# Performance work log

Measured on AMD Instinct MI355X. Metric: run time of the kernel, lower is better.

## Reference

```python
import jax, jax.numpy as jnp
import numpy as np

N_NODES = 100000
N_EDGES = 3200000
D_IN = 256
D_HID = 256
D_OUT = 64


def setup_inputs() -> dict:
    key = jax.random.key(0)
    k1, k2, k3, k4 = jax.random.split(key, 4)
    x = jax.random.normal(k1, (N_NODES, D_IN), dtype=jnp.float32)
    edge_index = jax.random.randint(k2, (2, N_EDGES), 0, N_NODES, dtype=jnp.int32)
    W1 = jax.random.normal(k3, (D_IN, D_HID), dtype=jnp.float32) / np.sqrt(D_IN)
    b1 = jnp.zeros((D_HID,), dtype=jnp.float32)
    W2 = jax.random.normal(k4, (D_HID, D_OUT), dtype=jnp.float32) / np.sqrt(D_HID)
    b2 = jnp.zeros((D_OUT,), dtype=jnp.float32)
    return {"x": x, "edge_index": edge_index, "W1": W1, "b1": b1, "W2": W2, "b2": b2}


def _gcn_conv(x, src, dst, norm, W, b, n_nodes):
    # dense linear transform, then normalized scatter-add aggregation
    h = x @ W  # [N, out]
    msg = norm[:, None] * h[src]  # gather + scale, [E+N, out]
    out = jax.ops.segment_sum(msg, dst, num_segments=n_nodes)
    return out + b


def reference(x, edge_index, W1, b1, W2, b2):
    n = x.shape[0]
    # add self-loops (PyG GCNConv default)
    loops = jnp.arange(n, dtype=edge_index.dtype)
    src = jnp.concatenate([edge_index[0], loops])
    dst = jnp.concatenate([edge_index[1], loops])
    # symmetric normalization deg^{-1/2}[src] * deg^{-1/2}[dst]
    deg = jax.ops.segment_sum(jnp.ones_like(src, dtype=x.dtype), dst, num_segments=n)
    dinv = jnp.where(deg > 0, jax.lax.rsqrt(jnp.maximum(deg, 1.0)), 0.0)
    norm = dinv[src] * dinv[dst]

    h = _gcn_conv(x, src, dst, norm, W1, b1, n)
    h = jax.nn.relu(h)
    # dropout is identity at inference
    h = _gcn_conv(h, src, dst, norm, W2, b2, n)
    return jax.nn.log_softmax(h, axis=1)
```

## Files before the change

kernel.cpp:

```cpp
#include <hip/hip_runtime.h>
#include <hip/hip_bf16.h>


typedef __bf16 bf16;
typedef bf16 bf16x8 __attribute__((ext_vector_type(8)));
typedef float f32x4 __attribute__((ext_vector_type(4)));
typedef float f32x2 __attribute__((ext_vector_type(2)));

#define NBLK 256

__global__ __launch_bounds__(256) void k_b1(const int* __restrict__ edge, int E, int chunk,
                                            int NB, int* __restrict__ gcnt) {
    __shared__ int cnt[512];
    int tid = threadIdx.x;
    for (int i = tid; i < NB; i += 256) cnt[i] = 0;
    __syncthreads();
    int s = blockIdx.x * chunk, e = min(s + chunk, E);
    for (int i = s + tid; i < e; i += 256) atomicAdd(&cnt[edge[E + i] >> 9], 1);
    __syncthreads();
    for (int i = tid; i < NB; i += 256) gcnt[blockIdx.x * NB + i] = cnt[i];
}

__global__ void k_b2(const int* __restrict__ gcnt, int NB, int E, int* __restrict__ bstart) {
    __shared__ int col[256];
    int k = threadIdx.x;
    int sum = 0;
    if (k < NB)
        for (int b = 0; b < NBLK; ++b) sum += gcnt[b * NB + k];
    col[k] = sum;
    __syncthreads();
    for (int o = 1; o < 256; o <<= 1) {
        int v = (k >= o) ? col[k - o] : 0;
        __syncthreads();
        col[k] += v;
        __syncthreads();
    }
    if (k < NB) bstart[k] = col[k] - sum;
    if (k == 0) bstart[NB] = E;
}

__global__ void k_b2b(int* __restrict__ gcnt, int NB, const int* __restrict__ bstart) {
    __shared__ int col[256];
    int b = threadIdx.x;
    int k = blockIdx.x;
    int v = gcnt[b * NB + k];
    col[b] = v;
    __syncthreads();
    for (int o = 1; o < 256; o <<= 1) {
        int t = (b >= o) ? col[b - o] : 0;
        __syncthreads();
        col[b] += t;
        __syncthreads();
    }
    gcnt[b * NB + k] = bstart[k] + col[b] - v;
}

__global__ __launch_bounds__(256) void k_b3(const int* __restrict__ edge, int E, int chunk,
                                            int NB, const int* __restrict__ base,
                                            int* __restrict__ ebuf) {
    __shared__ int cnt[512];
    __shared__ int bs[512];
    int tid = threadIdx.x;
    for (int i = tid; i < NB; i += 256) {
        cnt[i] = 0;
        bs[i] = base[blockIdx.x * NB + i];
    }
    __syncthreads();
    int s = blockIdx.x * chunk, e = min(s + chunk, E);
    for (int i = s + tid; i < e; i += 256) {
        int sv = edge[i], dv = edge[E + i];
        int k = dv >> 9;
        int r = atomicAdd(&cnt[k], 1);
        ebuf[bs[k] + r] = sv | ((dv & 511) << 17);
    }
}

__global__ __launch_bounds__(256) void k_b45(const int* __restrict__ ebuf,
                                             const int* __restrict__ bstart,
                                             const float* __restrict__ scale, int n, int E,
                                             int NB, int* __restrict__ off,
                                             float* __restrict__ dinv,
                                             float* __restrict__ ws) {
    __shared__ int cnt[512];
    __shared__ int red[256];
    int tid = threadIdx.x;
    int k = blockIdx.x;
    cnt[tid] = 0;
    cnt[tid + 256] = 0;
    __syncthreads();
    int s = bstart[k], e = bstart[k + 1];
    for (int i = s + tid; i < e; i += 256) atomicAdd(&cnt[(ebuf[i] >> 17) & 511], 1);
    __syncthreads();
    int c0 = cnt[tid * 2], c1 = cnt[tid * 2 + 1];
    int sum = c0 + c1;
    red[tid] = sum;
    __syncthreads();
    for (int o = 1; o < 256; o <<= 1) {
        int v = (tid >= o) ? red[tid - o] : 0;
        __syncthreads();
        red[tid] += v;
        __syncthreads();
    }
    int ex = red[tid] - sum;
    int base = k << 9;
    int g0 = base + tid * 2, g1 = g0 + 1;
    int o0 = s + ex, o1 = s + ex + c0;
    if (g0 < n) {
        off[g0] = o0;
        float d0 = rsqrtf((float)(c0 + 1));
        dinv[g0] = d0;
        ws[g0] = d0 * scale[g0];
    } else if (g0 == n) off[g0] = o0;
    if (g1 < n) {
        off[g1] = o1;
        float d1 = rsqrtf((float)(c1 + 1));
        dinv[g1] = d1;
        ws[g1] = d1 * scale[g1];
    } else if (g1 == n) off[g1] = o1;
    if (k == NB - 1 && tid == 0) off[n] = E;
}

__global__ __launch_bounds__(256) void k_b6(const int* __restrict__ ebuf,
                                            const int* __restrict__ bstart,
                                            const int* __restrict__ off,
                                            const float* __restrict__ ws, int n,
                                            int2* __restrict__ pair) {
    __shared__ int cnt[512];
    __shared__ int offl[512];
    int tid = threadIdx.x;
    int k = blockIdx.x;
    int base = k << 9;
    cnt[tid] = 0;
    cnt[tid + 256] = 0;
    offl[tid] = (base + tid < n) ? off[base + tid] : 0;
    offl[tid + 256] = (base + 256 + tid < n) ? off[base + 256 + tid] : 0;
    __syncthreads();
    int s = bstart[k], e = bstart[k + 1];
    for (int i = s + tid; i < e; i += 256) {
        int pk = ebuf[i];
        int sv = pk & 0x1ffff;
        int node = (pk >> 17) & 511;
        int r = atomicAdd(&cnt[node], 1);
        pair[offl[node] + r] = make_int2(sv << 8, __float_as_int(ws[sv]));
    }
}

__global__ __launch_bounds__(256) void k_quant(const float* __restrict__ x,
                                               unsigned char* __restrict__ xq,
                                               float* __restrict__ scale, int n) {
    int row = blockIdx.x * 4 + (threadIdx.x >> 6);
    int lane = threadIdx.x & 63;
    if (row >= n) return;
    f32x4 v = ((const f32x4*)x)[(size_t)row * 64 + lane];
    float m = fmaxf(fmaxf(fabsf(v[0]), fabsf(v[1])), fmaxf(fabsf(v[2]), fabsf(v[3])));
    for (int o = 32; o > 0; o >>= 1) m = fmaxf(m, __shfl_xor(m, o));
    m = fmaxf(m, 1e-20f);
    float inv = 127.0f / m;
    int b0 = (__float2int_rn(v[0] * inv) + 128) & 255;
    int b1 = (__float2int_rn(v[1] * inv) + 128) & 255;
    int b2 = (__float2int_rn(v[2] * inv) + 128) & 255;
    int b3 = (__float2int_rn(v[3] * inv) + 128) & 255;
    ((int*)xq)[(size_t)row * 64 + lane] = b0 | (b1 << 8) | (b2 << 16) | (b3 << 24);
    if (lane == 0) scale[row] = m / 127.0f;
}

__global__ __launch_bounds__(256) void k_quant2(const bf16* __restrict__ tb,
                                                const float* __restrict__ dinv,
                                                unsigned char* __restrict__ tq,
                                                float* __restrict__ w2v, int n) {
    int t = blockIdx.x * 256 + threadIdx.x;
    int row = t >> 3;
    int l8 = t & 7;
    if (row >= n) return;
    bf16x8 v = ((const bf16x8*)tb)[(size_t)row * 8 + l8];
    float f[8], m = 0.0f;
#pragma unroll
    for (int j = 0; j < 8; ++j) { f[j] = (float)v[j]; m = fmaxf(m, fabsf(f[j])); }
    for (int o = 4; o > 0; o >>= 1) m = fmaxf(m, __shfl_xor(m, o));
    m = fmaxf(m, 1e-20f);
    float inv = 127.0f / m;
    int lo = 0, hi = 0;
#pragma unroll
    for (int j = 0; j < 4; ++j) lo |= ((__float2int_rn(f[j] * inv) + 128) & 255) << (8 * j);
#pragma unroll
    for (int j = 0; j < 4; ++j) hi |= ((__float2int_rn(f[4 + j] * inv) + 128) & 255) << (8 * j);
    ((int2*)tq)[(size_t)row * 8 + l8] = make_int2(lo, hi);
    if (l8 == 0) w2v[row] = dinv[row] * (m / 127.0f);
}

__global__ void k_wt(const float* __restrict__ W, bf16* __restrict__ Wt, int NC) {
    int nc = blockIdx.x;
    int k = threadIdx.x;
    Wt[nc * 256 + k] = (bf16)W[k * NC + nc];
}

__device__ __forceinline__ void acc16(f32x2 a[8], uint4 t, float w, float& wsum) {
    wsum += w;
    f32x2 w2 = {w, w};
    unsigned u0 = t.x, u1 = t.y, u2 = t.z, u3 = t.w;
    f32x2 c;
    c[0] = (float)(u0 & 255u);         c[1] = (float)((u0 >> 8) & 255u);  a[0] += w2 * c;
    c[0] = (float)((u0 >> 16) & 255u); c[1] = (float)(u0 >> 24);         a[1] += w2 * c;
    c[0] = (float)(u1 & 255u);         c[1] = (float)((u1 >> 8) & 255u);  a[2] += w2 * c;
    c[0] = (float)((u1 >> 16) & 255u); c[1] = (float)(u1 >> 24);         a[3] += w2 * c;
    c[0] = (float)(u2 & 255u);         c[1] = (float)((u2 >> 8) & 255u);  a[4] += w2 * c;
    c[0] = (float)((u2 >> 16) & 255u); c[1] = (float)(u2 >> 24);         a[5] += w2 * c;
    c[0] = (float)(u3 & 255u);         c[1] = (float)((u3 >> 8) & 255u);  a[6] += w2 * c;
    c[0] = (float)((u3 >> 16) & 255u); c[1] = (float)(u3 >> 24);         a[7] += w2 * c;
}

__device__ __forceinline__ void acc8(f32x2 a[4], int2 t, float w, float& wsum) {
    wsum += w;
    f32x2 w2 = {w, w};
    unsigned u0 = (unsigned)t.x, u1 = (unsigned)t.y;
    f32x2 c;
    c[0] = (float)(u0 & 255u);         c[1] = (float)((u0 >> 8) & 255u);  a[0] += w2 * c;
    c[0] = (float)((u0 >> 16) & 255u); c[1] = (float)(u0 >> 24);         a[1] += w2 * c;
    c[0] = (float)(u1 & 255u);         c[1] = (float)((u1 >> 8) & 255u);  a[2] += w2 * c;
    c[0] = (float)((u1 >> 16) & 255u); c[1] = (float)(u1 >> 24);         a[3] += w2 * c;
}

__global__ __launch_bounds__(256) void k_agg1(const unsigned char* __restrict__ xq,
                                              const float* __restrict__ wsv,
                                              const int* __restrict__ off,
                                              const int2* __restrict__ pair,
                                              const float* __restrict__ dinv,
                                              bf16* __restrict__ ax, int n) {
    int wv = blockIdx.x * 4 + (threadIdx.x >> 6);
    int lane = threadIdx.x & 63;
    int node = wv * 4 + (lane >> 4);
    int l16 = lane & 15;
    if (node >= n) return;
    int s0 = off[node], s1 = off[node + 1];
    float dv = dinv[node];
    const unsigned char* xqb = xq + l16 * 16;
    f32x2 a[8] = {};
    float wsum = 0.0f;
    uint4 xs = *(const uint4*)(xqb + (size_t)node * 256);
    acc16(a, xs, wsv[node], wsum);
    int e = s0;
    if (s1 - s0 >= 8) {
        int2 p[8];
#pragma unroll
        for (int q = 0; q < 8; ++q) p[q] = pair[s0 + q];
        e = s0 + 8;
        for (; e + 8 <= s1; e += 8) {
            uint4 t[8];
#pragma unroll
            for (int q = 0; q < 8; ++q)
                t[q] = *(const uint4*)(xqb + (unsigned)p[q].x);
            int2 pn[8];
#pragma unroll
            for (int q = 0; q < 8; ++q) pn[q] = pair[e + q];
#pragma unroll
            for (int q = 0; q < 8; ++q) acc16(a, t[q], __int_as_float(p[q].y), wsum);
#pragma unroll
            for (int q = 0; q < 8; ++q) p[q] = pn[q];
        }
        uint4 t[8];
#pragma unroll
        for (int q = 0; q < 8; ++q)
            t[q] = *(const uint4*)(xqb + (unsigned)p[q].x);
#pragma unroll
        for (int q = 0; q < 8; ++q) acc16(a, t[q], __int_as_float(p[q].y), wsum);
    }
    for (; e < s1; ++e) {
        int2 p = pair[e];
        uint4 t = *(const uint4*)(xqb + (unsigned)p.x);
        acc16(a, t, __int_as_float(p.y), wsum);
    }
    float c = 128.0f * wsum;
    bf16x8 o0, o1;
#pragma unroll
    for (int j = 0; j < 4; ++j) {
        o0[2 * j]     = (bf16)((a[j][0] - c) * dv);
        o0[2 * j + 1] = (bf16)((a[j][1] - c) * dv);
        o1[2 * j]     = (bf16)((a[4 + j][0] - c) * dv);
        o1[2 * j + 1] = (bf16)((a[4 + j][1] - c) * dv);
    }
    ((bf16x8*)ax)[(size_t)node * 32 + l16 * 2] = o0;
    ((bf16x8*)ax)[(size_t)node * 32 + l16 * 2 + 1] = o1;
}

__device__ __forceinline__ int swz(int s) { return s ^ ((s >> 3) & 7); }

__global__ __launch_bounds__(256) void k_gemmp(const bf16* __restrict__ A,
                                               const bf16* __restrict__ Bt,
                                               const float* __restrict__ bias,
                                               bf16* __restrict__ C, int n) {
    __shared__ __align__(16) bf16 As[4 * 64 * 8];
    __shared__ __align__(16) bf16 Bs[16 * 64 * 8];
    int tid = threadIdx.x;
    int bm = blockIdx.x * 64;
    int w = tid >> 6, lane = tid & 63;

    int r = tid >> 2;
    int cq = tid & 3;
    int a_slot = swz(((r >> 4) * 64) + cq * 16 + (r & 15));
    int arow = bm + r; if (arow > n - 1) arow = n - 1;

    f32x4 acc[16] = {};

    for (int k0 = 0; k0 < 256; k0 += 32) {
        __syncthreads();
        uint4 av = *(const uint4*)(A + (size_t)arow * 256 + k0 + cq * 8);
        *(uint4*)(As + a_slot * 8) = av;
#pragma unroll
        for (int rep = 0; rep < 4; ++rep) {
            int r2 = rep * 64 + r;
            uint4 bv = *(const uint4*)(Bt + (size_t)r2 * 256 + k0 + cq * 8);
            *(uint4*)(Bs + swz(((r2 >> 4) * 64) + cq * 16 + (r2 & 15)) * 8) = bv;
        }
        __syncthreads();
        bf16x8 af = *(const bf16x8*)(As + swz(w * 64 + lane) * 8);
#pragma unroll
        for (int ct = 0; ct < 16; ++ct) {
            bf16x8 bfr = *(const bf16x8*)(Bs + swz(ct * 64 + lane) * 8);
            acc[ct] = __builtin_amdgcn_mfma_f32_16x16x32_bf16(af, bfr, acc[ct], 0, 0, 0);
        }
    }

    int colb = lane & 15, rowq = lane >> 4;
#pragma unroll
    for (int ct = 0; ct < 16; ++ct) {
        int col = ct * 16 + colb;
        float bv = bias[col];
#pragma unroll
        for (int rr = 0; rr < 4; ++rr) {
            int row = bm + w * 16 + rowq * 4 + rr;
            if (row < n) {
                float v = acc[ct][rr] + bv;
                C[(size_t)row * 256 + col] = (bf16)(v > 0.0f ? v : 0.0f);
            }
        }
    }
}

__global__ __launch_bounds__(256) void k_gemm2(const bf16* __restrict__ A,
                                               const bf16* __restrict__ Bt,
                                               bf16* __restrict__ C, int n) {
    __shared__ __align__(16) bf16 As[4 * 64 * 8];
    __shared__ __align__(16) bf16 Bs[4 * 64 * 8];
    int tid = threadIdx.x;
    int bm = blockIdx.x * 64;
    int w = tid >> 6, lane = tid & 63;
    int wm = w >> 1, wn = w & 1;

    int r = tid >> 2;
    int cq = tid & 3;
    int lds_slot = swz(((r >> 4) * 64) + cq * 16 + (r & 15));
    int arow = bm + r; if (arow > n - 1) arow = n - 1;

    f32x4 acc[2][2] = {};

    for (int k0 = 0; k0 < 256; k0 += 32) {
        __syncthreads();
        uint4 av = *(const uint4*)(A + (size_t)arow * 256 + k0 + cq * 8);
        uint4 bv = *(const uint4*)(Bt + (size_t)r * 256 + k0 + cq * 8);
        *(uint4*)(As + lds_slot * 8) = av;
        *(uint4*)(Bs + lds_slot * 8) = bv;
        __syncthreads();
#pragma unroll
        for (int i = 0; i < 2; ++i) {
            bf16x8 af = *(const bf16x8*)(As + swz((wm * 2 + i) * 64 + lane) * 8);
#pragma unroll
            for (int j = 0; j < 2; ++j) {
                bf16x8 bfr = *(const bf16x8*)(Bs + swz((wn * 2 + j) * 64 + lane) * 8);
                acc[i][j] = __builtin_amdgcn_mfma_f32_16x16x32_bf16(af, bfr, acc[i][j], 0, 0, 0);
            }
        }
    }

    int colb = lane & 15, rowq = lane >> 4;
#pragma unroll
    for (int i = 0; i < 2; ++i) {
#pragma unroll
        for (int j = 0; j < 2; ++j) {
            int col = wn * 32 + j * 16 + colb;
#pragma unroll
            for (int rr = 0; rr < 4; ++rr) {
                int row = bm + wm * 32 + i * 16 + rowq * 4 + rr;
                if (row < n) C[(size_t)row * 64 + col] = (bf16)acc[i][j][rr];
            }
        }
    }
}

__global__ __launch_bounds__(256) void k_agg2(const unsigned char* __restrict__ tq,
                                              const float* __restrict__ w2v,
                                              const int* __restrict__ off,
                                              const int2* __restrict__ pair,
                                              const float* __restrict__ dinv,
                                              const float* __restrict__ b2,
                                              float* __restrict__ out, int n) {
    int wv = blockIdx.x * 4 + (threadIdx.x >> 6);
    int lane = threadIdx.x & 63;
    int node = wv * 8 + (lane >> 3);
    int l8 = lane & 7;
    if (node >= n) return;
    int s0 = off[node], s1 = off[node + 1];
    float dv = dinv[node];
    const unsigned char* tqb = tq + l8 * 8;
    int2 ts = *(const int2*)(tqb + (size_t)node * 64);
    f32x2 a[4] = {};
    float wsum = 0.0f;
    acc8(a, ts, w2v[node], wsum);
    int e = s0;
    if (s1 - s0 >= 4) {
        int2 p[4]; float sc[4];
#pragma unroll
        for (int q = 0; q < 4; ++q) p[q] = pair[s0 + q];
#pragma unroll
        for (int q = 0; q < 4; ++q) sc[q] = w2v[(unsigned)p[q].x >> 8];
        e = s0 + 4;
        for (; e + 4 <= s1; e += 4) {
            int2 t[4];
#pragma unroll
            for (int q = 0; q < 4; ++q) t[q] = *(const int2*)(tqb + ((unsigned)p[q].x >> 2));
            int2 pn[4];
#pragma unroll
            for (int q = 0; q < 4; ++q) pn[q] = pair[e + q];
            float scn[4];
#pragma unroll
            for (int q = 0; q < 4; ++q) scn[q] = w2v[(unsigned)pn[q].x >> 8];
#pragma unroll
            for (int q = 0; q < 4; ++q) acc8(a, t[q], sc[q], wsum);
#pragma unroll
            for (int q = 0; q < 4; ++q) { p[q] = pn[q]; sc[q] = scn[q]; }
        }
        int2 t[4];
#pragma unroll
        for (int q = 0; q < 4; ++q) t[q] = *(const int2*)(tqb + ((unsigned)p[q].x >> 2));
#pragma unroll
        for (int q = 0; q < 4; ++q) acc8(a, t[q], sc[q], wsum);
    }
    for (; e < s1; ++e) {
        int2 p = pair[e];
        float w = w2v[(unsigned)p.x >> 8];
        int2 t = *(const int2*)(tqb + ((unsigned)p.x >> 2));
        acc8(a, t, w, wsum);
    }
    float c = 128.0f * wsum;
    float aa[8];
#pragma unroll
    for (int j = 0; j < 4; ++j) { aa[2 * j] = a[j][0]; aa[2 * j + 1] = a[j][1]; }
    const float4* B2 = (const float4*)b2;
    float4 bv0 = B2[l8 * 2], bv1 = B2[l8 * 2 + 1];
    aa[0] = (aa[0] - c) * dv + bv0.x; aa[1] = (aa[1] - c) * dv + bv0.y;
    aa[2] = (aa[2] - c) * dv + bv0.z; aa[3] = (aa[3] - c) * dv + bv0.w;
    aa[4] = (aa[4] - c) * dv + bv1.x; aa[5] = (aa[5] - c) * dv + bv1.y;
    aa[6] = (aa[6] - c) * dv + bv1.z; aa[7] = (aa[7] - c) * dv + bv1.w;
    float m = aa[0];
#pragma unroll
    for (int j = 1; j < 8; ++j) m = fmaxf(m, aa[j]);
    for (int o = 4; o > 0; o >>= 1) m = fmaxf(m, __shfl_xor(m, o));
    float s = 0.0f;
#pragma unroll
    for (int j = 0; j < 8; ++j) s += __expf(aa[j] - m);
    for (int o = 4; o > 0; o >>= 1) s += __shfl_xor(s, o);
    float ls = m + __logf(s);
    f32x4 o0, o1;
    o0[0] = aa[0] - ls; o0[1] = aa[1] - ls; o0[2] = aa[2] - ls; o0[3] = aa[3] - ls;
    o1[0] = aa[4] - ls; o1[1] = aa[5] - ls; o1[2] = aa[6] - ls; o1[3] = aa[7] - ls;
    f32x4* O = (f32x4*)out;
    O[(size_t)node * 16 + l8 * 2] = o0;
    O[(size_t)node * 16 + l8 * 2 + 1] = o1;
}

extern "C" void kernel_launch(void* const* d_in, const int* in_sizes, int n_in,
                              void* d_out, int out_size, void* d_ws, size_t ws_size,
                              hipStream_t stream) {
    const float* x   = (const float*)d_in[0];
    const int*  edge = (const int*)d_in[1];
    const float* W1  = (const float*)d_in[2];
    const float* b1  = (const float*)d_in[3];
    const float* W2  = (const float*)d_in[4];
    const float* b2  = (const float*)d_in[5];
    float* out = (float*)d_out;

    int n = in_sizes[0] / 256;
    int E = in_sizes[1] / 2;
    int NB = (n + 511) >> 9;
    int chunk = (E + NBLK - 1) / NBLK;

    char* ws = (char*)d_ws;
    auto alloc = [&](size_t bytes) -> char* {
        char* p = ws;
        ws += (bytes + 255) & ~(size_t)255;
        return p;
    };
    int*   gcnt   = (int*)alloc((size_t)NBLK * NB * 4);
    int*   bstart = (int*)alloc((size_t)(NB + 1) * 4);
    int*   ebuf   = (int*)alloc((size_t)E * 4);
    float* dinv   = (float*)alloc((size_t)n * 4);
    float* wsv    = (float*)alloc((size_t)n * 4);
    int*   off    = (int*)alloc((size_t)(n + 1) * 4);
    int2*  pair   = (int2*)alloc((size_t)E * 8);
    unsigned char* xq = (unsigned char*)alloc((size_t)n * 256);
    float* scale  = (float*)alloc((size_t)n * 4);
    bf16*  ax     = (bf16*)alloc((size_t)n * 256 * 2);
    bf16*  h1     = (bf16*)alloc((size_t)n * 256 * 2);
    bf16*  tb     = (bf16*)alloc((size_t)n * 64 * 2);
    unsigned char* tq = (unsigned char*)alloc((size_t)n * 64);
    float* w2v    = (float*)alloc((size_t)n * 4);
    bf16*  W1t    = (bf16*)alloc(256 * 256 * 2);
    bf16*  W2t    = (bf16*)alloc(64 * 256 * 2);

    k_quant<<<(n + 3) / 4, 256, 0, stream>>>(x, xq, scale, n);

    k_b1<<<NBLK, 256, 0, stream>>>(edge, E, chunk, NB, gcnt);
    k_b2<<<1, 256, 0, stream>>>(gcnt, NB, E, bstart);
    k_b2b<<<NB, 256, 0, stream>>>(gcnt, NB, bstart);
    k_b3<<<NBLK, 256, 0, stream>>>(edge, E, chunk, NB, gcnt, ebuf);
    k_b45<<<NB, 256, 0, stream>>>(ebuf, bstart, scale, n, E, NB, off, dinv, wsv);
    k_b6<<<NB, 256, 0, stream>>>(ebuf, bstart, off, wsv, n, pair);

    k_wt<<<256, 256, 0, stream>>>(W1, W1t, 256);
    k_wt<<<64, 256, 0, stream>>>(W2, W2t, 64);

    k_agg1<<<(n + 15) / 16, 256, 0, stream>>>(xq, wsv, off, pair, dinv, ax, n);
    k_gemmp<<<(n + 63) / 64, 256, 0, stream>>>(ax, W1t, b1, h1, n);

    k_gemm2<<<(n + 63) / 64, 256, 0, stream>>>(h1, W2t, tb, n);
    k_quant2<<<(n * 8 + 255) / 256, 256, 0, stream>>>(tb, dinv, tq, w2v, n);
    k_agg2<<<(n + 31) / 32, 256, 0, stream>>>(tq, w2v, off, pair, dinv, b2, out, n);
}
```

Measured before the change: 541.4 us.

## Retile layer-1 GEMM to 128-row blocks, deepen agg2 prefetch, merge weight transposes

The first GEMM now runs 512-thread blocks over 128 rows, and each wave computes a 64x64 output tile with a 4x4 MFMA register block, so LDS fragment loads are reused across more MFMAs. The layer-2 aggregation software pipeline is widened from 4 to 8 edges in flight to hide gather latency. The two weight-transpose launches are merged into one kernel. The changes raise register pressure in the GEMM and in agg2, which may lower occupancy, and nodes with fewer than 8 edges now go entirely through the scalar tail loop.

```diff
diff --git a/kernel.cpp b/kernel.cpp
--- a/kernel.cpp
+++ b/kernel.cpp
@@ -188,10 +188,12 @@
     if (l8 == 0) w2v[row] = dinv[row] * (m / 127.0f);
 }
 
-__global__ void k_wt(const float* __restrict__ W, bf16* __restrict__ Wt, int NC) {
-    int nc = blockIdx.x;
+__global__ void k_wt(const float* __restrict__ W1, const float* __restrict__ W2,
+                     bf16* __restrict__ W1t, bf16* __restrict__ W2t) {
+    int b = blockIdx.x;
     int k = threadIdx.x;
-    Wt[nc * 256 + k] = (bf16)W[k * NC + nc];
+    if (b < 256) W1t[b * 256 + k] = (bf16)W1[k * 256 + b];
+    else { int nc = b - 256; W2t[nc * 256 + k] = (bf16)W2[k * 64 + nc]; }
 }
 
 __device__ __forceinline__ void acc16(f32x2 a[8], uint4 t, float w, float& wsum) {
@@ -284,56 +286,66 @@
 
 __device__ __forceinline__ int swz(int s) { return s ^ ((s >> 3) & 7); }
 
-__global__ __launch_bounds__(256) void k_gemmp(const bf16* __restrict__ A,
+__global__ __launch_bounds__(512) void k_gemmp(const bf16* __restrict__ A,
                                                const bf16* __restrict__ Bt,
                                                const float* __restrict__ bias,
                                                bf16* __restrict__ C, int n) {
-    __shared__ __align__(16) bf16 As[4 * 64 * 8];
+    __shared__ __align__(16) bf16 As[8 * 64 * 8];
     __shared__ __align__(16) bf16 Bs[16 * 64 * 8];
     int tid = threadIdx.x;
-    int bm = blockIdx.x * 64;
+    int bm = blockIdx.x * 128;
     int w = tid >> 6, lane = tid & 63;
+    int wm = w >> 2;
+    int wn = w & 3;
 
     int r = tid >> 2;
     int cq = tid & 3;
     int a_slot = swz(((r >> 4) * 64) + cq * 16 + (r & 15));
     int arow = bm + r; if (arow > n - 1) arow = n - 1;
 
-    f32x4 acc[16] = {};
+    f32x4 acc[4][4] = {};
 
     for (int k0 = 0; k0 < 256; k0 += 32) {
         __syncthreads();
         uint4 av = *(const uint4*)(A + (size_t)arow * 256 + k0 + cq * 8);
         *(uint4*)(As + a_slot * 8) = av;
 #pragma unroll
-        for (int rep = 0; rep < 4; ++rep) {
-            int r2 = rep * 64 + r;
+        for (int rep = 0; rep < 2; ++rep) {
+            int r2 = rep * 128 + r;
             uint4 bv = *(const uint4*)(Bt + (size_t)r2 * 256 + k0 + cq * 8);
             *(uint4*)(Bs + swz(((r2 >> 4) * 64) + cq * 16 + (r2 & 15)) * 8) = bv;
         }
         __syncthreads();
-        bf16x8 af = *(const bf16x8*)(As + swz(w * 64 + lane) * 8);
-#pragma unroll
-        for (int ct = 0; ct < 16; ++ct) {
-            bf16x8 bfr = *(const bf16x8*)(Bs + swz(ct * 64 + lane) * 8);
-            acc[ct] = __builtin_amdgcn_mfma_f32_16x16x32_bf16(af, bfr, acc[ct], 0, 0, 0);
-        }
+        bf16x8 af[4], bfr[4];
+#pragma unroll
+        for (int i = 0; i < 4; ++i)
+            af[i] = *(const bf16x8*)(As + swz(((wm * 4 + i) * 64) + lane) * 8);
+#pragma unroll
+        for (int j = 0; j < 4; ++j)
+            bfr[j] = *(const bf16x8*)(Bs + swz(((wn * 4 + j) * 64) + lane) * 8);
+#pragma unroll
+        for (int i = 0; i < 4; ++i)
+#pragma unroll
+            for (int j = 0; j < 4; ++j)
+                acc[i][j] = __builtin_amdgcn_mfma_f32_16x16x32_bf16(af[i], bfr[j], acc[i][j], 0, 0, 0);
     }
 
     int colb = lane & 15, rowq = lane >> 4;
 #pragma unroll
-    for (int ct = 0; ct < 16; ++ct) {
-        int col = ct * 16 + colb;
-        float bv = bias[col];
-#pragma unroll
-        for (int rr = 0; rr < 4; ++rr) {
-            int row = bm + w * 16 + rowq * 4 + rr;
-            if (row < n) {
-                float v = acc[ct][rr] + bv;
-                C[(size_t)row * 256 + col] = (bf16)(v > 0.0f ? v : 0.0f);
+    for (int i = 0; i < 4; ++i)
+#pragma unroll
+        for (int j = 0; j < 4; ++j) {
+            int col = wn * 64 + j * 16 + colb;
+            float bv = bias[col];
+#pragma unroll
+            for (int rr = 0; rr < 4; ++rr) {
+                int row = bm + wm * 64 + i * 16 + rowq * 4 + rr;
+                if (row < n) {
+                    float v = acc[i][j][rr] + bv;
+                    C[(size_t)row * 256 + col] = (bf16)(v > 0.0f ? v : 0.0f);
+                }
             }
         }
-    }
 }
 
 __global__ __launch_bounds__(256) void k_gemm2(const bf16* __restrict__ A,
@@ -406,33 +418,33 @@
     float wsum = 0.0f;
     acc8(a, ts, w2v[node], wsum);
     int e = s0;
-    if (s1 - s0 >= 4) {
-        int2 p[4]; float sc[4];
-#pragma unroll
-        for (int q = 0; q < 4; ++q) p[q] = pair[s0 + q];
-#pragma unroll
-        for (int q = 0; q < 4; ++q) sc[q] = w2v[(unsigned)p[q].x >> 8];
-        e = s0 + 4;
-        for (; e + 4 <= s1; e += 4) {
-            int2 t[4];
-#pragma unroll
-            for (int q = 0; q < 4; ++q) t[q] = *(const int2*)(tqb + ((unsigned)p[q].x >> 2));
-            int2 pn[4];
-#pragma unroll
-            for (int q = 0; q < 4; ++q) pn[q] = pair[e + q];
-            float scn[4];
-#pragma unroll
-            for (int q = 0; q < 4; ++q) scn[q] = w2v[(unsigned)pn[q].x >> 8];
-#pragma unroll
-            for (int q = 0; q < 4; ++q) acc8(a, t[q], sc[q], wsum);
-#pragma unroll
-            for (int q = 0; q < 4; ++q) { p[q] = pn[q]; sc[q] = scn[q]; }
+    if (s1 - s0 >= 8) {
+        int2 p[8]; float sc[8];
+#pragma unroll
+        for (int q = 0; q < 8; ++q) p[q] = pair[s0 + q];
+#pragma unroll
+        for (int q = 0; q < 8; ++q) sc[q] = w2v[(unsigned)p[q].x >> 8];
+        e = s0 + 8;
+        for (; e + 8 <= s1; e += 8) {
+            int2 t[8];
+#pragma unroll
+            for (int q = 0; q < 8; ++q) t[q] = *(const int2*)(tqb + ((unsigned)p[q].x >> 2));
+            int2 pn[8];
+#pragma unroll
+            for (int q = 0; q < 8; ++q) pn[q] = pair[e + q];
+            float scn[8];
+#pragma unroll
+            for (int q = 0; q < 8; ++q) scn[q] = w2v[(unsigned)pn[q].x >> 8];
+#pragma unroll
+            for (int q = 0; q < 8; ++q) acc8(a, t[q], sc[q], wsum);
+#pragma unroll
+            for (int q = 0; q < 8; ++q) { p[q] = pn[q]; sc[q] = scn[q]; }
         }
-        int2 t[4];
-#pragma unroll
-        for (int q = 0; q < 4; ++q) t[q] = *(const int2*)(tqb + ((unsigned)p[q].x >> 2));
-#pragma unroll
-        for (int q = 0; q < 4; ++q) acc8(a, t[q], sc[q], wsum);
+        int2 t[8];
+#pragma unroll
+        for (int q = 0; q < 8; ++q) t[q] = *(const int2*)(tqb + ((unsigned)p[q].x >> 2));
+#pragma unroll
+        for (int q = 0; q < 8; ++q) acc8(a, t[q], sc[q], wsum);
     }
     for (; e < s1; ++e) {
         int2 p = pair[e];
@@ -515,11 +527,10 @@
     k_b45<<<NB, 256, 0, stream>>>(ebuf, bstart, scale, n, E, NB, off, dinv, wsv);
     k_b6<<<NB, 256, 0, stream>>>(ebuf, bstart, off, wsv, n, pair);
 
-    k_wt<<<256, 256, 0, stream>>>(W1, W1t, 256);
-    k_wt<<<64, 256, 0, stream>>>(W2, W2t, 64);
+    k_wt<<<320, 256, 0, stream>>>(W1, W2, W1t, W2t);
 
     k_agg1<<<(n + 15) / 16, 256, 0, stream>>>(xq, wsv, off, pair, dinv, ax, n);
-    k_gemmp<<<(n + 63) / 64, 256, 0, stream>>>(ax, W1t, b1, h1, n);
+    k_gemmp<<<(n + 127) / 128, 512, 0, stream>>>(ax, W1t, b1, h1, n);
 
     k_gemm2<<<(n + 63) / 64, 256, 0, stream>>>(h1, W2t, tb, n);
     k_quant2<<<(n * 8 + 255) / 256, 256, 0, stream>>>(tb, dinv, tq, w2v, n);
```

Measured after the change: 521.1 us. 1.04x faster.
